# Optimization experiments

Hardware: AMD Instinct MI355X
Metric: run time of the kernel (lower is better)

## Reference

```python
import jax, jax.numpy as jnp
import numpy as np

N = 1024      # hidden_nodes (number of columns)
W = 128       # column_width
D = 1024      # input_dimension
F = W * N + N # per-column i-layer input size
SPARSITY = W / (W * (N - 1) + N) * 1.0  # modified_sparsity with total_neigbours=1


def setup_inputs() -> dict:
    key = jax.random.key(0)
    ks = jax.random.split(key, 10)
    s = lambda fan_in: 1.0 / np.sqrt(fan_in)
    x = jax.random.normal(ks[0], (D,), jnp.float32)
    hidden_state = jax.random.normal(ks[1], (N,), jnp.float32)
    W1 = jax.random.uniform(ks[2], (N, W, D), jnp.float32, -s(D), s(D))
    b1 = jax.random.uniform(ks[3], (N, W), jnp.float32, -s(D), s(D))
    W2 = jax.random.uniform(ks[4], (N, W, W), jnp.float32, -s(W), s(W))
    b2 = jax.random.uniform(ks[5], (N, W), jnp.float32, -s(W), s(W))
    Wi = jax.random.uniform(ks[6], (N, F), jnp.float32, -s(F), s(F))
    bi = jax.random.uniform(ks[7], (N,), jnp.float32, -s(F), s(F))
    # bernoulli mask, then force each column's own width-block to 1
    mask = (jax.random.uniform(ks[8], (N, F), jnp.float32) < SPARSITY).astype(jnp.float32)
    cols = jnp.arange(F)
    owner = jnp.where(cols < N * W, cols // W, -1)          # which column owns each feature slot
    block = (owner[None, :] == jnp.arange(N)[:, None]).astype(jnp.float32)
    mask = jnp.maximum(mask, block)
    pred = 0.1 * jax.random.normal(ks[9], (N,), jnp.float32)  # prediction_parameters ~ N(0, 0.1)
    return {"x": x, "hidden_state": hidden_state, "W1": W1, "b1": b1,
            "W2": W2, "b2": b2, "Wi": Wi, "bi": bi, "mask": mask, "pred": pred}


def reference(x, hidden_state, W1, b1, W2, b2, Wi, bi, mask, pred):
    # phase 1: per-column feature extractor (fc1 -> relu -> fc2 -> relu), batched over columns
    f1 = jax.nn.relu(jnp.einsum('nwd,d->nw', W1, x) + b1)        # [N, W]
    f2 = jax.nn.relu(jnp.einsum('nvw,nw->nv', W2, f1) + b2)      # [N, W]
    # phase 2: every column sees concat(all features, all hidden states)
    feat = jnp.concatenate([f2.reshape(-1), hidden_state])       # [F] = [N*W + N]
    i = jnp.tanh(jnp.einsum('nf,f->n', Wi * mask, feat) + bi)    # [N]
    h = hidden_state + i                                         # [N]
    y = jnp.sum(pred * h)                                        # scalar prediction
    return y, h
```

## Files before the change

### kernel.cpp

```cpp
#include <hip/hip_runtime.h>
#include <math.h>

#define NN 1024
#define WW 128
#define DD 1024
#define FF (NN * WW + NN)
#define NROW (NN * WW)
#define NCHUNK 516
#define NWORD (NCHUNK * 4)
#define GWAVES 8192

#define WS_BM_OFF  528384
#define WS_F1_OFF  (WS_BM_OFF + (size_t)NN * NWORD * 8)
#define WS_NEEDED  (WS_F1_OFF + (size_t)NROW * 4)

typedef float f32x4 __attribute__((ext_vector_type(4)));
typedef float f32x2 __attribute__((ext_vector_type(2)));

__device__ __forceinline__ f32x4 nt4(const float* p) {
    return __builtin_nontemporal_load(reinterpret_cast<const f32x4*>(p));
}
__device__ __forceinline__ float wred(float s) {
    #pragma unroll
    for (int m = 32; m > 0; m >>= 1) s += __shfl_xor(s, m, 64);
    return s;
}
__device__ __forceinline__ float hred(float s) {
    #pragma unroll
    for (int m = 16; m > 0; m >>= 1) s += __shfl_xor(s, m, 64);
    return s;
}

__global__ __launch_bounds__(256) void w1dot(
    const float* __restrict__ x, const float* __restrict__ W1,
    const float* __restrict__ b1, float* __restrict__ f1)
{
    const int tid = threadIdx.x, lane = tid & 63;
    const int gw = blockIdx.x * 4 + (tid >> 6);

    const f32x4 xv0 = *reinterpret_cast<const f32x4*>(x +   0 + lane * 4);
    const f32x4 xv1 = *reinterpret_cast<const f32x4*>(x + 256 + lane * 4);
    const f32x4 xv2 = *reinterpret_cast<const f32x4*>(x + 512 + lane * 4);
    const f32x4 xv3 = *reinterpret_cast<const f32x4*>(x + 768 + lane * 4);

    #pragma unroll
    for (int i = 0; i < 8; ++i) {
        const int r = (i * GWAVES + gw) * 2;
        const float* rp = W1 + (size_t)r * DD + lane * 4;
        f32x4 a0 = nt4(rp) * xv0;
        f32x4 a1 = nt4(rp + DD) * xv0;
        a0 += nt4(rp + 256) * xv1;
        a1 += nt4(rp + DD + 256) * xv1;
        a0 += nt4(rp + 512) * xv2;
        a1 += nt4(rp + DD + 512) * xv2;
        a0 += nt4(rp + 768) * xv3;
        a1 += nt4(rp + DD + 768) * xv3;
        float s0 = wred((a0[0] + a0[1]) + (a0[2] + a0[3]));
        float s1 = wred((a1[0] + a1[1]) + (a1[2] + a1[3]));
        if (lane == 0) {
            const float v0 = s0 + b1[r];
            const float v1 = s1 + b1[r + 1];
            f1[r]     = v0 > 0.f ? v0 : 0.f;
            f1[r + 1] = v1 > 0.f ? v1 : 0.f;
        }
    }
}

__global__ __launch_bounds__(256) void w2dot(
    const float* __restrict__ W2, const float* __restrict__ b2,
    const float* __restrict__ f1, const float* __restrict__ hidden,
    float* __restrict__ feat)
{
    const int tid = threadIdx.x, lane = tid & 63;
    const int gw = blockIdx.x * 4 + (tid >> 6);
    const int gtid = blockIdx.x * 256 + tid;
    if (gtid < NN) feat[NROW + gtid] = hidden[gtid];

    #pragma unroll
    for (int i = 0; i < 8; ++i) {
        const int p  = i * GWAVES + gw;
        const int rr = p * 2;
        const int n  = p >> 6;
        const f32x4 wv = nt4(W2 + (size_t)p * 256 + lane * 4);
        const f32x4 fv = *reinterpret_cast<const f32x4*>(f1 + (n << 7) + ((lane & 31) << 2));
        const f32x4 m = wv * fv;
        const float s = hred((m[0] + m[1]) + (m[2] + m[3]));
        if (lane == 0) {
            const float v = s + b2[rr];
            feat[rr] = v > 0.f ? v : 0.f;
        } else if (lane == 32) {
            const float v = s + b2[rr + 1];
            feat[rr + 1] = v > 0.f ? v : 0.f;
        }
    }
}

__global__ __launch_bounds__(256) void maskscan(
    const float* __restrict__ mask, unsigned long long* __restrict__ bm)
{
    const int tid = threadIdx.x, lane = tid & 63, w = tid >> 6;
    const int wave_id = blockIdx.x * 4 + w;
    const int nwaves  = gridDim.x * 4;
    const int total   = NN * NCHUNK;
    #pragma unroll 2
    for (int c = wave_id; c < total; c += nwaves) {
        const f32x4 m = nt4(mask + (size_t)c * 256 + lane * 4);
        const unsigned long long q0 = __ballot(m[0] != 0.f);
        const unsigned long long q1 = __ballot(m[1] != 0.f);
        const unsigned long long q2 = __ballot(m[2] != 0.f);
        const unsigned long long q3 = __ballot(m[3] != 0.f);
        if (lane < 4) {
            const unsigned long long v = lane == 0 ? q0 : lane == 1 ? q1 : lane == 2 ? q2 : q3;
            bm[(size_t)c * 4 + lane] = v;
        }
    }
}

__global__ __launch_bounds__(256) void dotk(
    const unsigned long long* __restrict__ bm, const float* __restrict__ Wi,
    const float* __restrict__ feat, const float* __restrict__ bi,
    const float* __restrict__ hidden, float* __restrict__ out)
{
    const int n = blockIdx.x, tid = threadIdx.x;
    const unsigned long long* brow = bm + (size_t)n * NWORD;
    const float* wrow = Wi + (size_t)n * FF;
    float acc = 0.f;
    for (int wd = tid; wd < NWORD; wd += 256) {
        unsigned long long q = brow[wd];
        const int basef = (wd >> 2) * 256 + (wd & 3);
        while (q) {
            const int l = __builtin_ctzll(q);
            const int f = basef + l * 4;
            acc += wrow[f] * feat[f];
            q &= q - 1;
        }
    }
    acc = wred(acc);
    __shared__ float partial[4];
    if ((tid & 63) == 0) partial[tid >> 6] = acc;
    __syncthreads();
    if (tid == 0) {
        const float s = (partial[0] + partial[1]) + (partial[2] + partial[3]);
        out[1 + n] = hidden[n] + tanhf(s + bi[n]);
    }
}

__global__ __launch_bounds__(256) void predk(
    const float* __restrict__ pred, const float* __restrict__ h,
    float* __restrict__ out)
{
    const int tid = threadIdx.x;
    float acc = 0.f;
    for (int i = tid; i < NN; i += 256) acc += pred[i] * h[i];
    acc = wred(acc);
    __shared__ float partial[4];
    if ((tid & 63) == 0) partial[tid >> 6] = acc;
    __syncthreads();
    if (tid == 0) out[0] = (partial[0] + partial[1]) + (partial[2] + partial[3]);
}

__global__ __launch_bounds__(256) void feat_kernel(
    const float* __restrict__ x, const float* __restrict__ hidden,
    const float* __restrict__ W1, const float* __restrict__ b1,
    const float* __restrict__ W2, const float* __restrict__ b2,
    float* __restrict__ feat)
{
    const int n = blockIdx.x, tid = threadIdx.x, lane = tid & 63, wave = tid >> 6;
    __shared__ float x_s[DD];
    __shared__ float f1_s[WW];
    *reinterpret_cast<float4*>(x_s + tid * 4) = *reinterpret_cast<const float4*>(x + tid * 4);
    if (tid == 0) feat[NROW + n] = hidden[n];
    __syncthreads();
    const float* W1n = W1 + (size_t)n * WW * DD;
    for (int r = wave * 32; r < wave * 32 + 32; ++r) {
        const float* row = W1n + (size_t)r * DD;
        float4 acc = {0.f, 0.f, 0.f, 0.f};
        #pragma unroll
        for (int it = 0; it < 4; ++it) {
            const float4 a  = *reinterpret_cast<const float4*>(row + it * 256 + lane * 4);
            const float4 xv = *reinterpret_cast<const float4*>(x_s + it * 256 + lane * 4);
            acc.x += a.x * xv.x; acc.y += a.y * xv.y;
            acc.z += a.z * xv.z; acc.w += a.w * xv.w;
        }
        float s = wred((acc.x + acc.y) + (acc.z + acc.w));
        if (lane == 0) {
            float v = s + b1[n * WW + r];
            f1_s[r] = v > 0.f ? v : 0.f;
        }
    }
    __syncthreads();
    const float* W2n = W2 + (size_t)n * WW * WW;
    for (int r = wave * 32; r < wave * 32 + 32; ++r) {
        const float2 a = *reinterpret_cast<const float2*>(W2n + (size_t)r * WW + lane * 2);
        const float2 f = *reinterpret_cast<const float2*>(f1_s + lane * 2);
        float s = wred(a.x * f.x + a.y * f.y);
        if (lane == 0) {
            float v = s + b2[n * WW + r];
            feat[n * WW + r] = v > 0.f ? v : 0.f;
        }
    }
}

__global__ __launch_bounds__(256) void sparse_kernel(
    const float* __restrict__ Wi, const float* __restrict__ mask,
    const float* __restrict__ bi, const float* __restrict__ hidden,
    const float* __restrict__ feat, float* __restrict__ out)
{
    const int n = blockIdx.x, tid = threadIdx.x;
    const float* mrow = mask + (size_t)n * FF;
    const float* wrow = Wi   + (size_t)n * FF;
    float acc = 0.f;
    for (int it = 0; it < FF / 1024; ++it) {
        const int f = it * 1024 + tid * 4;
        const float4 m = *reinterpret_cast<const float4*>(mrow + f);
        if (m.x != 0.f) acc += wrow[f + 0] * m.x * feat[f + 0];
        if (m.y != 0.f) acc += wrow[f + 1] * m.y * feat[f + 1];
        if (m.z != 0.f) acc += wrow[f + 2] * m.z * feat[f + 2];
        if (m.w != 0.f) acc += wrow[f + 3] * m.w * feat[f + 3];
    }
    acc = wred(acc);
    __shared__ float partial[4];
    if ((tid & 63) == 0) partial[tid >> 6] = acc;
    __syncthreads();
    if (tid == 0) {
        const float s = (partial[0] + partial[1]) + (partial[2] + partial[3]);
        out[1 + n] = hidden[n] + tanhf(s + bi[n]);
    }
}

extern "C" void kernel_launch(void* const* d_in, const int* in_sizes, int n_in,
                              void* d_out, int out_size, void* d_ws, size_t ws_size,
                              hipStream_t stream) {
    const float* x      = (const float*)d_in[0];
    const float* hidden = (const float*)d_in[1];
    const float* W1     = (const float*)d_in[2];
    const float* b1     = (const float*)d_in[3];
    const float* W2     = (const float*)d_in[4];
    const float* b2     = (const float*)d_in[5];
    const float* Wi     = (const float*)d_in[6];
    const float* bi     = (const float*)d_in[7];
    const float* mask   = (const float*)d_in[8];
    const float* pred   = (const float*)d_in[9];

    float* out  = (float*)d_out;
    float* feat = (float*)d_ws;
    unsigned long long* bm = (unsigned long long*)((char*)d_ws + WS_BM_OFF);
    float* f1 = (float*)((char*)d_ws + WS_F1_OFF);

    if (ws_size >= WS_NEEDED) {
        w1dot<<<2048, 256, 0, stream>>>(x, W1, b1, f1);
        w2dot<<<2048, 256, 0, stream>>>(W2, b2, f1, hidden, feat);
        maskscan<<<2048, 256, 0, stream>>>(mask, bm);
        dotk<<<NN, 256, 0, stream>>>(bm, Wi, feat, bi, hidden, out);
    } else {
        feat_kernel<<<NN, 256, 0, stream>>>(x, hidden, W1, b1, W2, b2, feat);
        sparse_kernel<<<NN, 256, 0, stream>>>(Wi, mask, bi, hidden, feat, out);
    }
    predk<<<1, 256, 0, stream>>>(pred, out + 1, out);
}
```

Baseline: 211.7 us.

## Fuse mask scan with sparse Wi gather into per-chunk partial sums

Replaces the two-pass scheme, which built a bitmask from the mask and then had a per-row kernel walk its bits, with a single wide kernel. That kernel reads each 256-element mask chunk, gathers Wi·feat for the nonzero entries on the spot, and writes one partial sum per chunk. A small follow-up kernel sums the 516 partials per row and applies tanh. This drops the bitmask write/read round trip and the serial per-thread bit loop, which had poor parallelism with one block per row. The cost is a wave reduction for every chunk, including empty ones, plus a partials buffer and scattered Wi loads issued from the streaming kernel.

```diff
diff --git a/kernel.cpp b/kernel.cpp
--- a/kernel.cpp
+++ b/kernel.cpp
@@ -7,15 +7,13 @@
 #define FF (NN * WW + NN)
 #define NROW (NN * WW)
 #define NCHUNK 516
-#define NWORD (NCHUNK * 4)
 #define GWAVES 8192
 
-#define WS_BM_OFF  528384
-#define WS_F1_OFF  (WS_BM_OFF + (size_t)NN * NWORD * 8)
-#define WS_NEEDED  (WS_F1_OFF + (size_t)NROW * 4)
+#define WS_F1_OFF   528384
+#define WS_PART_OFF (WS_F1_OFF + (size_t)NROW * 4)
+#define WS_NEEDED   (WS_PART_OFF + (size_t)NN * NCHUNK * 4)
 
 typedef float f32x4 __attribute__((ext_vector_type(4)));
-typedef float f32x2 __attribute__((ext_vector_type(2)));
 
 __device__ __forceinline__ f32x4 nt4(const float* p) {
     return __builtin_nontemporal_load(reinterpret_cast<const f32x4*>(p));
@@ -37,12 +35,10 @@
 {
     const int tid = threadIdx.x, lane = tid & 63;
     const int gw = blockIdx.x * 4 + (tid >> 6);
-
     const f32x4 xv0 = *reinterpret_cast<const f32x4*>(x +   0 + lane * 4);
     const f32x4 xv1 = *reinterpret_cast<const f32x4*>(x + 256 + lane * 4);
     const f32x4 xv2 = *reinterpret_cast<const f32x4*>(x + 512 + lane * 4);
     const f32x4 xv3 = *reinterpret_cast<const f32x4*>(x + 768 + lane * 4);
-
     #pragma unroll
     for (int i = 0; i < 8; ++i) {
         const int r = (i * GWAVES + gw) * 2;
@@ -75,7 +71,6 @@
     const int gw = blockIdx.x * 4 + (tid >> 6);
     const int gtid = blockIdx.x * 256 + tid;
     if (gtid < NN) feat[NROW + gtid] = hidden[gtid];
-
     #pragma unroll
     for (int i = 0; i < 8; ++i) {
         const int p  = i * GWAVES + gw;
@@ -95,52 +90,44 @@
     }
 }
 
-__global__ __launch_bounds__(256) void maskscan(
-    const float* __restrict__ mask, unsigned long long* __restrict__ bm)
+__global__ __launch_bounds__(256) void scangather(
+    const float* __restrict__ mask, const float* __restrict__ Wi,
+    const float* __restrict__ feat, float* __restrict__ partial)
 {
     const int tid = threadIdx.x, lane = tid & 63, w = tid >> 6;
     const int wave_id = blockIdx.x * 4 + w;
-    const int nwaves  = gridDim.x * 4;
-    const int total   = NN * NCHUNK;
     #pragma unroll 2
-    for (int c = wave_id; c < total; c += nwaves) {
+    for (int c = wave_id; c < NN * NCHUNK; c += GWAVES) {
         const f32x4 m = nt4(mask + (size_t)c * 256 + lane * 4);
-        const unsigned long long q0 = __ballot(m[0] != 0.f);
-        const unsigned long long q1 = __ballot(m[1] != 0.f);
-        const unsigned long long q2 = __ballot(m[2] != 0.f);
-        const unsigned long long q3 = __ballot(m[3] != 0.f);
-        if (lane < 4) {
-            const unsigned long long v = lane == 0 ? q0 : lane == 1 ? q1 : lane == 2 ? q2 : q3;
-            bm[(size_t)c * 4 + lane] = v;
-        }
-    }
-}
-
-__global__ __launch_bounds__(256) void dotk(
-    const unsigned long long* __restrict__ bm, const float* __restrict__ Wi,
-    const float* __restrict__ feat, const float* __restrict__ bi,
+        float a = 0.f;
+        if ((m[0] != 0.f) || (m[1] != 0.f) || (m[2] != 0.f) || (m[3] != 0.f)) {
+            const int n  = c / NCHUNK;
+            const int fl = (c - n * NCHUNK) * 256 + lane * 4;
+            const float* wrow = Wi + (size_t)n * FF;
+            if (m[0] != 0.f) a += wrow[fl]     * feat[fl];
+            if (m[1] != 0.f) a += wrow[fl + 1] * feat[fl + 1];
+            if (m[2] != 0.f) a += wrow[fl + 2] * feat[fl + 2];
+            if (m[3] != 0.f) a += wrow[fl + 3] * feat[fl + 3];
+        }
+        const float s = wred(a);
+        if (lane == 0) partial[c] = s;
+    }
+}
+
+__global__ __launch_bounds__(256) void sumk(
+    const float* __restrict__ partial, const float* __restrict__ bi,
     const float* __restrict__ hidden, float* __restrict__ out)
 {
     const int n = blockIdx.x, tid = threadIdx.x;
-    const unsigned long long* brow = bm + (size_t)n * NWORD;
-    const float* wrow = Wi + (size_t)n * FF;
+    const float* prow = partial + (size_t)n * NCHUNK;
     float acc = 0.f;
-    for (int wd = tid; wd < NWORD; wd += 256) {
-        unsigned long long q = brow[wd];
-        const int basef = (wd >> 2) * 256 + (wd & 3);
-        while (q) {
-            const int l = __builtin_ctzll(q);
-            const int f = basef + l * 4;
-            acc += wrow[f] * feat[f];
-            q &= q - 1;
-        }
-    }
+    for (int j = tid; j < NCHUNK; j += 256) acc += prow[j];
     acc = wred(acc);
-    __shared__ float partial[4];
-    if ((tid & 63) == 0) partial[tid >> 6] = acc;
+    __shared__ float p4[4];
+    if ((tid & 63) == 0) p4[tid >> 6] = acc;
     __syncthreads();
     if (tid == 0) {
-        const float s = (partial[0] + partial[1]) + (partial[2] + partial[3]);
+        const float s = (p4[0] + p4[1]) + (p4[2] + p4[3]);
         out[1 + n] = hidden[n] + tanhf(s + bi[n]);
     }
 }
@@ -153,10 +140,10 @@
     float acc = 0.f;
     for (int i = tid; i < NN; i += 256) acc += pred[i] * h[i];
     acc = wred(acc);
-    __shared__ float partial[4];
-    if ((tid & 63) == 0) partial[tid >> 6] = acc;
-    __syncthreads();
-    if (tid == 0) out[0] = (partial[0] + partial[1]) + (partial[2] + partial[3]);
+    __shared__ float p4[4];
+    if ((tid & 63) == 0) p4[tid >> 6] = acc;
+    __syncthreads();
+    if (tid == 0) out[0] = (p4[0] + p4[1]) + (p4[2] + p4[3]);
 }
 
 __global__ __launch_bounds__(256) void feat_kernel(
@@ -219,11 +206,11 @@
         if (m.w != 0.f) acc += wrow[f + 3] * m.w * feat[f + 3];
     }
     acc = wred(acc);
-    __shared__ float partial[4];
-    if ((tid & 63) == 0) partial[tid >> 6] = acc;
+    __shared__ float p4[4];
+    if ((tid & 63) == 0) p4[tid >> 6] = acc;
     __syncthreads();
     if (tid == 0) {
-        const float s = (partial[0] + partial[1]) + (partial[2] + partial[3]);
+        const float s = (p4[0] + p4[1]) + (p4[2] + p4[3]);
         out[1 + n] = hidden[n] + tanhf(s + bi[n]);
     }
 }
@@ -242,16 +229,16 @@
     const float* mask   = (const float*)d_in[8];
     const float* pred   = (const float*)d_in[9];
 
-    float* out  = (float*)d_out;
-    float* feat = (float*)d_ws;
-    unsigned long long* bm = (unsigned long long*)((char*)d_ws + WS_BM_OFF);
-    float* f1 = (float*)((char*)d_ws + WS_F1_OFF);
+    float* out     = (float*)d_out;
+    float* feat    = (float*)d_ws;
+    float* f1      = (float*)((char*)d_ws + WS_F1_OFF);
+    float* partial = (float*)((char*)d_ws + WS_PART_OFF);
 
     if (ws_size >= WS_NEEDED) {
         w1dot<<<2048, 256, 0, stream>>>(x, W1, b1, f1);
         w2dot<<<2048, 256, 0, stream>>>(W2, b2, f1, hidden, feat);
-        maskscan<<<2048, 256, 0, stream>>>(mask, bm);
-        dotk<<<NN, 256, 0, stream>>>(bm, Wi, feat, bi, hidden, out);
+        scangather<<<2048, 256, 0, stream>>>(mask, Wi, feat, partial);
+        sumk<<<NN, 256, 0, stream>>>(partial, bi, hidden, out);
     } else {
         feat_kernel<<<NN, 256, 0, stream>>>(x, hidden, W1, b1, W2, b2, feat);
         sparse_kernel<<<NN, 256, 0, stream>>>(Wi, mask, bi, hidden, feat, out);
```

New measurement: 202.3 us. 4.5% less time.
